# Performance work log

Measured on AMD Instinct MI355X. Metric: run time of the kernel, lower is better.

Reference implementation:

```python
import jax, jax.numpy as jnp
import numpy as np

S, B, T = 512, 512, 64


def setup_inputs() -> dict:
    key = jax.random.key(0)
    k1, k2, k3, k4, k5 = jax.random.split(key, 5)
    emissions = jax.random.normal(k1, (S, B, T), dtype=jnp.float32)
    tags = jax.random.randint(k2, (S, B), 0, T, dtype=jnp.int64)
    mask = jnp.ones((S, B), dtype=jnp.bool_)
    # parameters: uniform(-0.1, 0.1) as in _reset_parameters
    start_transitions = jax.random.uniform(k3, (T,), minval=-0.1, maxval=0.1, dtype=jnp.float32)
    end_transitions = jax.random.uniform(k4, (T,), minval=-0.1, maxval=0.1, dtype=jnp.float32)
    transitions = jax.random.uniform(k5, (T, T), minval=-0.1, maxval=0.1, dtype=jnp.float32)
    return {
        "emissions": emissions,
        "tags": tags,
        "mask": mask,
        "start_transitions": start_transitions,
        "end_transitions": end_transitions,
        "transitions": transitions,
    }


def _crf_llh(emissions, tags, mask, start_transitions, end_transitions, transitions):
    # emissions: [S, B, T]; tags: [S, B] int; mask: [S, B] bool (time-major)
    s, b_sz, _ = emissions.shape
    b = jnp.arange(b_sz)
    maskf = mask.astype(emissions.dtype)

    # ----- numerator: score of the given tag path -----
    score = start_transitions[tags[0]] + emissions[0, b, tags[0]]  # [B]
    trans_step = transitions[tags[:-1], tags[1:]]                  # [S-1, B]
    em_step = jnp.take_along_axis(emissions, tags[..., None], axis=2)[..., 0]  # [S, B]
    score = score + jnp.sum((trans_step + em_step[1:]) * maskf[1:], axis=0)
    seq_ends = mask.astype(jnp.int32).sum(axis=0) - 1              # [B]
    last_tags = tags[seq_ends, b]
    numerator = score + end_transitions[last_tags]                 # [B]

    # ----- denominator: forward-algorithm log partition -----
    def step(alpha, xs):
        em_i, m_i = xs  # [B, T], [B]
        # alpha[b, i] + transitions[i, j] + em_i[b, j] -> logsumexp over i
        nxt = jax.nn.logsumexp(alpha[:, :, None] + transitions[None, :, :] + em_i[:, None, :], axis=1)
        return jnp.where(m_i[:, None], nxt, alpha), None

    alpha0 = start_transitions + emissions[0]  # [B, T]
    alpha, _ = jax.lax.scan(step, alpha0, (emissions[1:], mask[1:]))
    denominator = jax.nn.logsumexp(alpha + end_transitions, axis=1)  # [B]

    llh = numerator - denominator
    return llh.mean()  # reduction='mean' (the default)


def reference(emissions, tags, mask, start_transitions, end_transitions, transitions):
    return _crf_llh(emissions, tags, mask, start_transitions, end_transitions, transitions)
```

## Files before the change

### kernel.cpp

```cpp
#include <hip/hip_runtime.h>
#include <math.h>

#define SS 512
#define BB 512
#define TT 64
#define GRP 8

typedef float vf16 __attribute__((ext_vector_type(16)));
typedef float vf8  __attribute__((ext_vector_type(8)));
typedef int   vi8  __attribute__((ext_vector_type(8)));

__device__ __forceinline__ float bl0(float x) {
    return __int_as_float(__builtin_amdgcn_readfirstlane(__float_as_int(x)));
}
__device__ __forceinline__ float rlane(float x, int i) {
    return __int_as_float(__builtin_amdgcn_readlane(__float_as_int(x), i));
}

__device__ __forceinline__ float matvec64(float p, vf16 eA, vf16 eB, vf16 eC, vf16 eD) {
    float a0 = 0.f, a1 = 0.f, a2 = 0.f, a3 = 0.f;
    #pragma unroll
    for (int i = 0; i < 16; ++i) {
        a0 = fmaf(rlane(p, i     ), eA[i], a0);
        a1 = fmaf(rlane(p, i + 16), eB[i], a1);
        a2 = fmaf(rlane(p, i + 32), eC[i], a2);
        a3 = fmaf(rlane(p, i + 48), eD[i], a3);
    }
    return (a0 + a1) + (a2 + a3);
}

__device__ __forceinline__ float renorm(float sel, int& Lexp) {
    int bits = __float_as_int(bl0(sel)) & 0x7f800000;
    bits = bits < 0x00800000 ? 0x00800000 : bits;
    bits = bits > 0x7e800000 ? 0x7e800000 : bits;
    Lexp += (bits >> 23) - 127;
    float scale = __int_as_float(0x7f000000 - bits);
    return sel * scale;
}

#define LOADF(EV, MV, g) do {                                              \
    const int sb_ = 1 + (g) * GRP;                                         \
    _Pragma("unroll")                                                      \
    for (int k_ = 0; k_ < GRP; ++k_) {                                     \
        EV[k_] = embase[(size_t)(sb_ + k_) * BB * TT];                     \
        MV[k_] = mkbase[(sb_ + k_) * BB];                                  \
    } } while (0)

#define STEPSF(EV, MV, lastg) do {                                         \
    vf8 Em_;                                                               \
    _Pragma("unroll")                                                      \
    for (int k_ = 0; k_ < GRP; ++k_) Em_[k_] = __expf(EV[k_]);             \
    _Pragma("unroll")                                                      \
    for (int k_ = 0; k_ < GRP; ++k_) {                                     \
        float acc_ = matvec64(p, eA, eB, eC, eD);                          \
        float t_   = acc_ * Em_[k_];                                       \
        int   mk_  = MV[k_];                                               \
        if (k_ == GRP - 1) mk_ = (lastg) ? 0 : mk_;  \
        float sel_ = mk_ ? t_ : p;                                         \
        p = renorm(sel_, Lexp);                                            \
    } } while (0)

#define LOADB(EV, MV, g) do {                                              \
    const int sb_ = 511 - (g) * GRP;                                       \
    _Pragma("unroll")                                                      \
    for (int k_ = 0; k_ < GRP; ++k_) {                                     \
        EV[k_] = embase[(size_t)(sb_ - k_) * BB * TT];                     \
        MV[k_] = mkbase[(sb_ - k_) * BB];                                  \
    } } while (0)

#define STEPSB(EV, MV) do {                                                \
    vf8 Em_;                                                               \
    _Pragma("unroll")                                                      \
    for (int k_ = 0; k_ < GRP; ++k_) Em_[k_] = __expf(EV[k_]);             \
    _Pragma("unroll")                                                      \
    for (int k_ = 0; k_ < GRP; ++k_) {                                     \
        float u_   = q * Em_[k_];                                          \
        float acc_ = matvec64(u_, eA, eB, eC, eD);                         \
        float sel_ = MV[k_] ? acc_ : q;                                    \
        q = renorm(sel_, Lexp);                                            \
    } } while (0)

__global__ __launch_bounds__(64, 1) void crf_chains(
    const float* __restrict__ em,
    const int*   __restrict__ tags,
    const int*   __restrict__ mask,
    const float* __restrict__ start_t,
    const float* __restrict__ end_t,
    const float* __restrict__ trans,
    float* __restrict__ alpha_mid,
    float* __restrict__ beta_mid,
    float* __restrict__ num_ws)
{
    const int lane = threadIdx.x;
    const int bid  = blockIdx.x;
    __shared__ float lds[TT * 65];

    if (bid < BB) {
        const int b = bid;
        const float* embase = em + (size_t)b * TT + lane;
        const int*   mkbase = mask + b;

        vf16 eA, eB, eC, eD;
        #pragma unroll
        for (int i = 0; i < 16; ++i) {
            eA[i] = __expf(trans[(i     ) * TT + lane]);
            eB[i] = __expf(trans[(i + 16) * TT + lane]);
            eC[i] = __expf(trans[(i + 32) * TT + lane]);
            eD[i] = __expf(trans[(i + 48) * TT + lane]);
        }

        float av    = start_t[lane] + embase[0];
        float Lbase = bl0(av);
        float p     = __expf(av - Lbase);
        int   Lexp  = 0;

        vf8 em0, em1;
        vi8 mk0, mk1;

        LOADF(em0, mk0, 0);
        LOADF(em1, mk1, 1);
        for (int gg = 0; gg < 32; gg += 2) {
            STEPSF(em0, mk0, false);
            LOADF(em0, mk0, gg + 2);
            STEPSF(em1, mk1, gg + 1 == 31);
            LOADF(em1, mk1, gg + 3);
        }
        double a = (double)Lbase + (double)Lexp * 0.6931471805599453 + (double)__logf(p);
        alpha_mid[(size_t)b * TT + lane] = (float)a;

    } else if (bid < 2 * BB) {
        const int b = bid - BB;
        const float* embase = em + (size_t)b * TT + lane;
        const int*   mkbase = mask + b;

        for (int k = 0; k < TT; ++k)
            lds[k * 65 + lane] = trans[k * TT + lane];
        vf16 eA, eB, eC, eD;
        #pragma unroll
        for (int j = 0; j < 16; ++j) {
            eA[j] = __expf(lds[lane * 65 + j     ]);
            eB[j] = __expf(lds[lane * 65 + j + 16]);
            eC[j] = __expf(lds[lane * 65 + j + 32]);
            eD[j] = __expf(lds[lane * 65 + j + 48]);
        }

        float q    = __expf(end_t[lane]);
        int   Lexp = 0;

        vf8 em0, em1;
        vi8 mk0, mk1;

        LOADB(em0, mk0, 0);
        LOADB(em1, mk1, 1);
        for (int gg = 0; gg < 32; gg += 2) {
            STEPSB(em0, mk0);
            LOADB(em0, mk0, gg + 2);
            STEPSB(em1, mk1);
            LOADB(em1, mk1, gg + 3);
        }
        double bsum = (double)Lexp * 0.6931471805599453 + (double)__logf(q);
        beta_mid[(size_t)b * TT + lane] = (float)bsum;

    } else {
        const int b = bid - 2 * BB;
        float local = 0.f;
        int   mcnt  = 0;
        for (int s = lane; s < SS; s += 64) {
            int tag = tags[s * BB + b];
            int mk  = mask[s * BB + b];
            mcnt += mk;
            if (s == 0) {
                local += start_t[tag] + em[(size_t)b * TT + tag];
            } else if (mk) {
                int tp = tags[(s - 1) * BB + b];
                local += trans[tp * TT + tag] + em[(size_t)s * BB * TT + (size_t)b * TT + tag];
            }
        }
        #pragma unroll
        for (int d = 32; d > 0; d >>= 1) {
            local += __shfl_down(local, d, 64);
            mcnt  += __shfl_down(mcnt, d, 64);
        }
        if (lane == 0) {
            int last = tags[(mcnt - 1) * BB + b];
            num_ws[b] = local + end_t[last];
        }
    }
}

__global__ __launch_bounds__(512) void crf_llh(
    const float* __restrict__ alpha_mid,
    const float* __restrict__ beta_mid,
    const float* __restrict__ num_ws,
    float* __restrict__ llh)
{
    const int lane = threadIdx.x & 63;
    const int b    = blockIdx.x * 8 + (threadIdx.x >> 6);
    float v = alpha_mid[(size_t)b * TT + lane] + beta_mid[(size_t)b * TT + lane];
    float mx = v;
    #pragma unroll
    for (int d = 32; d > 0; d >>= 1) mx = fmaxf(mx, __shfl_xor(mx, d, 64));
    float s = __expf(v - mx);
    #pragma unroll
    for (int d = 32; d > 0; d >>= 1) s += __shfl_xor(s, d, 64);
    if (lane == 0) llh[b] = num_ws[b] - (mx + __logf(s));
}

__global__ __launch_bounds__(512) void crf_mean(const float* __restrict__ llh,
                                               float* __restrict__ out)
{
    const int t = threadIdx.x;
    float v = llh[t];
    #pragma unroll
    for (int d = 32; d > 0; d >>= 1) v += __shfl_down(v, d, 64);
    __shared__ float red[8];
    if ((t & 63) == 0) red[t >> 6] = v;
    __syncthreads();
    if (t == 0) {
        float s = 0.f;
        #pragma unroll
        for (int w = 0; w < 8; ++w) s += red[w];
        out[0] = s / (float)BB;
    }
}

extern "C" void kernel_launch(void* const* d_in, const int* in_sizes, int n_in,
                              void* d_out, int out_size, void* d_ws, size_t ws_size,
                              hipStream_t stream) {
    const float* em    = (const float*)d_in[0];
    const int*   tags  = (const int*)d_in[1];
    const int*   mask  = (const int*)d_in[2];
    const float* st    = (const float*)d_in[3];
    const float* en    = (const float*)d_in[4];
    const float* tr    = (const float*)d_in[5];

    float* ws        = (float*)d_ws;
    float* alpha_mid = ws;
    float* beta_mid  = ws + (size_t)BB * TT;
    float* num_ws    = ws + (size_t)2 * BB * TT;
    float* llh       = ws + (size_t)2 * BB * TT + BB;

    crf_chains<<<3 * BB, 64, 0, stream>>>(em, tags, mask, st, en, tr,
                                          alpha_mid, beta_mid, num_ws);
    crf_llh<<<BB / 8, 512, 0, stream>>>(alpha_mid, beta_mid, num_ws, llh);
    crf_mean<<<1, 512, 0, stream>>>(llh, (float*)d_out);
}
```

Measured before the change: 155.4 us.

## Replace readlane-based 64-wide matvec with ds_swizzle broadcast and half-wave exchange

The per-step 64x64 matvec previously broadcast each lane's value with 64 readlane instructions. These are scalar and serialize on the SALU-to-VALU path. It now uses 32 ds_swizzle broadcasts within each 32-lane half. Each lane accumulates partial sums for itself and for its partner lane in the other half, and a single shfl_xor across 32 combines them. The transition tables are re-laid out per half-wave, and the backward branch drops its LDS transpose. The trade is fewer broadcast ops on the serial critical path against LDS-unit swizzle latency and an extra cross-half shuffle per step.

```diff
diff --git a/kernel.cpp b/kernel.cpp
--- a/kernel.cpp
+++ b/kernel.cpp
@@ -12,21 +12,6 @@
 
 __device__ __forceinline__ float bl0(float x) {
     return __int_as_float(__builtin_amdgcn_readfirstlane(__float_as_int(x)));
-}
-__device__ __forceinline__ float rlane(float x, int i) {
-    return __int_as_float(__builtin_amdgcn_readlane(__float_as_int(x), i));
-}
-
-__device__ __forceinline__ float matvec64(float p, vf16 eA, vf16 eB, vf16 eC, vf16 eD) {
-    float a0 = 0.f, a1 = 0.f, a2 = 0.f, a3 = 0.f;
-    #pragma unroll
-    for (int i = 0; i < 16; ++i) {
-        a0 = fmaf(rlane(p, i     ), eA[i], a0);
-        a1 = fmaf(rlane(p, i + 16), eB[i], a1);
-        a2 = fmaf(rlane(p, i + 32), eC[i], a2);
-        a3 = fmaf(rlane(p, i + 48), eD[i], a3);
-    }
-    return (a0 + a1) + (a2 + a3);
 }
 
 __device__ __forceinline__ float renorm(float sel, int& Lexp) {
@@ -38,6 +23,32 @@
     return sel * scale;
 }
 
+__device__ __forceinline__ float swz_matvec(float x,
+    const vf16& e1a, const vf16& e1b, const vf16& e2a, const vf16& e2b)
+{
+    const int xi = __float_as_int(x);
+    float c0 = 0.f, c1 = 0.f, c2 = 0.f, c3 = 0.f;
+    float d0 = 0.f, d1 = 0.f, d2 = 0.f, d3 = 0.f;
+#define SWZFMA(I, CC, DD, EV1, EV2, K) do {                                   \
+    float b_ = __int_as_float(__builtin_amdgcn_ds_swizzle(xi, (I) << 5));     \
+    CC = fmaf(b_, EV1[K], CC);                                                \
+    DD = fmaf(b_, EV2[K], DD); } while (0)
+#define SWZ8(B, CC, DD, EV1, EV2, KB)                                          \
+    SWZFMA(B + 0, CC, DD, EV1, EV2, KB + 0); SWZFMA(B + 1, CC, DD, EV1, EV2, KB + 1); \
+    SWZFMA(B + 2, CC, DD, EV1, EV2, KB + 2); SWZFMA(B + 3, CC, DD, EV1, EV2, KB + 3); \
+    SWZFMA(B + 4, CC, DD, EV1, EV2, KB + 4); SWZFMA(B + 5, CC, DD, EV1, EV2, KB + 5); \
+    SWZFMA(B + 6, CC, DD, EV1, EV2, KB + 6); SWZFMA(B + 7, CC, DD, EV1, EV2, KB + 7)
+    SWZ8(0,  c0, d0, e1a, e2a, 0);
+    SWZ8(8,  c1, d1, e1a, e2a, 8);
+    SWZ8(16, c2, d2, e1b, e2b, 0);
+    SWZ8(24, c3, d3, e1b, e2b, 8);
+#undef SWZ8
+#undef SWZFMA
+    float c = (c0 + c1) + (c2 + c3);
+    float d = (d0 + d1) + (d2 + d3);
+    return c + __shfl_xor(d, 32, 64);
+}
+
 #define LOADF(EV, MV, g) do {                                              \
     const int sb_ = 1 + (g) * GRP;                                         \
     _Pragma("unroll")                                                      \
@@ -52,7 +63,7 @@
     for (int k_ = 0; k_ < GRP; ++k_) Em_[k_] = __expf(EV[k_]);             \
     _Pragma("unroll")                                                      \
     for (int k_ = 0; k_ < GRP; ++k_) {                                     \
-        float acc_ = matvec64(p, eA, eB, eC, eD);                          \
+        float acc_ = swz_matvec(p, e1a, e1b, e2a, e2b);                    \
         float t_   = acc_ * Em_[k_];                                       \
         int   mk_  = MV[k_];                                               \
         if (k_ == GRP - 1) mk_ = (lastg) ? 0 : mk_;  \
@@ -75,7 +86,7 @@
     _Pragma("unroll")                                                      \
     for (int k_ = 0; k_ < GRP; ++k_) {                                     \
         float u_   = q * Em_[k_];                                          \
-        float acc_ = matvec64(u_, eA, eB, eC, eD);                         \
+        float acc_ = swz_matvec(u_, e1a, e1b, e2a, e2b);                   \
         float sel_ = MV[k_] ? acc_ : q;                                    \
         q = renorm(sel_, Lexp);                                            \
     } } while (0)
@@ -93,20 +104,20 @@
 {
     const int lane = threadIdx.x;
     const int bid  = blockIdx.x;
-    __shared__ float lds[TT * 65];
+    const int hi   = lane & 32;
 
     if (bid < BB) {
         const int b = bid;
         const float* embase = em + (size_t)b * TT + lane;
         const int*   mkbase = mask + b;
 
-        vf16 eA, eB, eC, eD;
+        vf16 e1a, e1b, e2a, e2b;
         #pragma unroll
         for (int i = 0; i < 16; ++i) {
-            eA[i] = __expf(trans[(i     ) * TT + lane]);
-            eB[i] = __expf(trans[(i + 16) * TT + lane]);
-            eC[i] = __expf(trans[(i + 32) * TT + lane]);
-            eD[i] = __expf(trans[(i + 48) * TT + lane]);
+            e1a[i] = __expf(trans[(i      + hi) * TT + lane]);
+            e1b[i] = __expf(trans[(i + 16 + hi) * TT + lane]);
+            e2a[i] = __expf(trans[(i      + hi) * TT + (lane ^ 32)]);
+            e2b[i] = __expf(trans[(i + 16 + hi) * TT + (lane ^ 32)]);
         }
 
         float av    = start_t[lane] + embase[0];
@@ -133,15 +144,13 @@
         const float* embase = em + (size_t)b * TT + lane;
         const int*   mkbase = mask + b;
 
-        for (int k = 0; k < TT; ++k)
-            lds[k * 65 + lane] = trans[k * TT + lane];
-        vf16 eA, eB, eC, eD;
+        vf16 e1a, e1b, e2a, e2b;
         #pragma unroll
         for (int j = 0; j < 16; ++j) {
-            eA[j] = __expf(lds[lane * 65 + j     ]);
-            eB[j] = __expf(lds[lane * 65 + j + 16]);
-            eC[j] = __expf(lds[lane * 65 + j + 32]);
-            eD[j] = __expf(lds[lane * 65 + j + 48]);
+            e1a[j] = __expf(trans[lane * TT        + (j      + hi)]);
+            e1b[j] = __expf(trans[lane * TT        + (j + 16 + hi)]);
+            e2a[j] = __expf(trans[(lane ^ 32) * TT + (j      + hi)]);
+            e2b[j] = __expf(trans[(lane ^ 32) * TT + (j + 16 + hi)]);
         }
 
         float q    = __expf(end_t[lane]);
```

Result: slower. 167.5 us (+7.8%).
